# Kernel tuning notes

Measured on AMD Instinct MI355X. Metric: run time of the kernel, lower is better.

Reference implementation:

```python
import jax, jax.numpy as jnp
import numpy as np

B, F, V, E = 16384, 20, 100000, 32
D_BOT = F * E            # 640
DIMS = (512, 256)        # bottom MLP dims
TDIMS = (128, 64)        # tower hidden dims
N_DOM = 4


def setup_inputs() -> dict:
    key = jax.random.key(0)
    ks = jax.random.split(key, 16)
    inp = {
        "feature_ids": jax.random.randint(ks[0], (B, F), 0, V, dtype=jnp.int64),
        "domain_id": jax.random.randint(ks[1], (B,), 0, N_DOM, dtype=jnp.int64),
        # embedding tables [F, V, E]
        "emb": jax.random.normal(ks[2], (F, V, E), dtype=jnp.float32) * 0.01,
        # bottom MLP: 640 -> 512 -> 256 (relu, no output layer)
        "W1": jax.random.normal(ks[3], (D_BOT, DIMS[0]), dtype=jnp.float32) * (1.0 / np.sqrt(D_BOT)),
        "b1": jnp.zeros((DIMS[0],), dtype=jnp.float32),
        "W2": jax.random.normal(ks[4], (DIMS[0], DIMS[1]), dtype=jnp.float32) * (1.0 / np.sqrt(DIMS[0])),
        "b2": jnp.zeros((DIMS[1],), dtype=jnp.float32),
        # towers (stacked over domain dim): 256 -> 128 -> 64 -> 1
        "TW1": jax.random.normal(ks[5], (N_DOM, DIMS[1], TDIMS[0]), dtype=jnp.float32) * (1.0 / np.sqrt(DIMS[1])),
        "Tb1": jnp.zeros((N_DOM, TDIMS[0]), dtype=jnp.float32),
        "TW2": jax.random.normal(ks[6], (N_DOM, TDIMS[0], TDIMS[1]), dtype=jnp.float32) * (1.0 / np.sqrt(TDIMS[0])),
        "Tb2": jnp.zeros((N_DOM, TDIMS[1]), dtype=jnp.float32),
        "TW3": jax.random.normal(ks[7], (N_DOM, TDIMS[1], 1), dtype=jnp.float32) * (1.0 / np.sqrt(TDIMS[1])),
        "Tb3": jnp.zeros((N_DOM, 1), dtype=jnp.float32),
    }
    return inp


def reference(feature_ids, domain_id, emb, W1, b1, W2, b2, TW1, Tb1, TW2, Tb2, TW3, Tb3):
    # Embedding lookup + concat: [B, F, E] -> [B, F*E]
    e = emb[jnp.arange(F)[None, :], feature_ids]          # [B, F, E]
    h = e.reshape(B, F * E)
    # Shared bottom MLP (relu)
    h = jax.nn.relu(h @ W1 + b1)                          # [B, 512]
    h = jax.nn.relu(h @ W2 + b2)                          # [B, 256]
    # All domain towers computed densely for every sample (faithful to source)
    t = jax.nn.relu(jnp.einsum('bi,dio->bdo', h, TW1) + Tb1[None])   # [B, D, 128]
    t = jax.nn.relu(jnp.einsum('bdi,dio->bdo', t, TW2) + Tb2[None])  # [B, D, 64]
    logit = jnp.einsum('bdi,dio->bdo', t, TW3) + Tb3[None]           # [B, D, 1]
    ys = jax.nn.sigmoid(logit)[..., 0]                    # [B, D]
    # Select per-sample domain output via mask (domains are exclusive)
    onehot = jax.nn.one_hot(domain_id, N_DOM, dtype=ys.dtype)        # [B, D]
    final = jnp.sum(ys * onehot, axis=1)                  # [B]
    return final
```

## Files before the change

### kernel.cpp

```cpp
#include <hip/hip_runtime.h>

#define B_SZ  16384
#define F_SZ  20
#define V_SZ  100000
#define E_SZ  32
#define DBOT  640
#define D1    512
#define D2    256
#define T1D   128
#define T2D   64
#define NDOM  4

typedef __bf16 bf16x8 __attribute__((ext_vector_type(8)));
typedef float  f32x4  __attribute__((ext_vector_type(4)));

#define MFMA(a, b, c) __builtin_amdgcn_mfma_f32_16x16x32_bf16((a), (b), (c), 0, 0, 0)

__global__ __launch_bounds__(256) void k_prep(const float* __restrict__ W1,
                                              const float* __restrict__ W2,
                                              const float* __restrict__ TW1,
                                              const float* __restrict__ TW2,
                                              __bf16* __restrict__ W1P,
                                              __bf16* __restrict__ W2P,
                                              __bf16* __restrict__ TW1P,
                                              __bf16* __restrict__ TW2P) {
  int bid = blockIdx.x, tid = threadIdx.x;
  const float* src; __bf16* dst; int n, k, N;
  if (bid < 160) {
    long g = (long)bid * 256 + tid;
    int lane = g & 63; int kkg = (int)((g >> 6) % 20); int ntile = (int)(g / 1280);
    n = ntile * 16 + (lane & 15); k = kkg * 32 + ((lane >> 4) << 3);
    src = W1; N = D1; dst = W1P + g * 8;
  } else if (bid < 224) {
    long g = (long)(bid - 160) * 256 + tid;
    int lane = g & 63; int kkg = (int)((g >> 6) & 15); int ntile = (int)(g >> 10);
    n = ntile * 16 + (lane & 15); k = kkg * 32 + ((lane >> 4) << 3);
    src = W2; N = D2; dst = W2P + g * 8;
  } else if (bid < 288) {
    long g = (long)(bid - 224) * 256 + tid;
    int d = (int)(g >> 12); long r = g & 4095;
    int lane = r & 63; int kkg = (int)((r >> 6) & 7); int ntile = (int)(r >> 9);
    n = ntile * 16 + (lane & 15); k = kkg * 32 + ((lane >> 4) << 3);
    src = TW1 + (long)d * D2 * T1D; N = T1D;
    dst = TW1P + ((long)(d * 64 + ntile * 8 + kkg) * 64 + lane) * 8;
  } else {
    long g = (long)(bid - 288) * 256 + tid;
    int d = (int)(g >> 10); long r = g & 1023;
    int lane = r & 63; int kkg = (int)((r >> 6) & 3); int ntile = (int)(r >> 8);
    n = ntile * 16 + (lane & 15); k = kkg * 32 + ((lane >> 4) << 3);
    src = TW2 + (long)d * T1D * T2D; N = T2D;
    dst = TW2P + ((long)(d * 16 + ntile * 4 + kkg) * 64 + lane) * 8;
  }
  bf16x8 o;
#pragma unroll
  for (int e = 0; e < 8; ++e) o[e] = (__bf16)src[(long)(k + e) * N + n];
  *(bf16x8*)dst = o;
}

__global__ __launch_bounds__(512) void k_mega(const int* __restrict__ fids,
                                              const int* __restrict__ dom,
                                              const float* __restrict__ emb,
                                              const __bf16* __restrict__ W1P,
                                              const float* __restrict__ b1,
                                              const __bf16* __restrict__ W2P,
                                              const float* __restrict__ b2,
                                              const __bf16* __restrict__ TW1P,
                                              const __bf16* __restrict__ TW2P,
                                              const float* __restrict__ Tb1,
                                              const float* __restrict__ Tb2,
                                              const float* __restrict__ TW3,
                                              const float* __restrict__ Tb3,
                                              float* __restrict__ out) {
  __shared__ __attribute__((aligned(16))) char smem[152576];
  int*    ids_lds = (int*)(smem + 147456);
  __bf16* sA      = (__bf16*)smem;
  __bf16* h1      = (__bf16*)(smem + 81920);
  __bf16* h2_lds  = (__bf16*)smem;
  __bf16* t_lds   = (__bf16*)(smem + 81920);

  int bid = blockIdx.x, tid = threadIdx.x;
  int lane = tid & 63, w = tid >> 6;
  int lrow = lane & 15, kq = lane >> 4;
  int m0 = bid * 64;

  for (int i = tid; i < 64 * F_SZ; i += 512) ids_lds[i] = fids[m0 * F_SZ + i];
  __syncthreads();

  int row0 = tid >> 4,          cc0 = tid & 15;
  int row1 = (tid + 512) >> 4,  cc1 = tid & 15;
  int sb0 = (row0 * 1280 + cc0 * 16) ^ ((row0 & 7) << 4);
  int sb1 = (row1 * 1280 + cc1 * 16) ^ ((row1 & 7) << 4);
  int f0base = cc0 >> 2, es0 = (cc0 & 3) << 3;
  int f1base = cc1 >> 2, es1 = (cc1 & 3) << 3;

  float4 g0a, g0b, g1a, g1b;
  {
    int f = f0base;
    int id = ids_lds[row0 * F_SZ + f];
    const float* p = emb + ((long)f * V_SZ + id) * E_SZ + es0;
    g0a = *(const float4*)p; g0b = *(const float4*)(p + 4);
    f = f1base;
    id = ids_lds[row1 * F_SZ + f];
    const float* q = emb + ((long)f * V_SZ + id) * E_SZ + es1;
    g1a = *(const float4*)q; g1b = *(const float4*)(q + 4);
  }

  f32x4 acc[4][4] = {};

#pragma unroll
  for (int g = 0; g < 5; ++g) {
    {
      bf16x8 o;
      o[0] = (__bf16)g0a.x; o[1] = (__bf16)g0a.y; o[2] = (__bf16)g0a.z; o[3] = (__bf16)g0a.w;
      o[4] = (__bf16)g0b.x; o[5] = (__bf16)g0b.y; o[6] = (__bf16)g0b.z; o[7] = (__bf16)g0b.w;
      *(bf16x8*)((char*)sA + sb0 + g * 256) = o;
      o[0] = (__bf16)g1a.x; o[1] = (__bf16)g1a.y; o[2] = (__bf16)g1a.z; o[3] = (__bf16)g1a.w;
      o[4] = (__bf16)g1b.x; o[5] = (__bf16)g1b.y; o[6] = (__bf16)g1b.z; o[7] = (__bf16)g1b.w;
      *(bf16x8*)((char*)sA + sb1 + g * 256) = o;
    }
    asm volatile("s_waitcnt lgkmcnt(0)" ::: "memory");
    __builtin_amdgcn_s_barrier();
    __builtin_amdgcn_sched_barrier(0);

    bf16x8 bfr[4][4];
#pragma unroll
    for (int f4 = 0; f4 < 4; ++f4)
#pragma unroll
      for (int ni = 0; ni < 4; ++ni)
        bfr[f4][ni] = *(const bf16x8*)(W1P +
            ((long)((w * 4 + ni) * 20 + g * 4 + f4) * 64 + lane) * 8);
    __builtin_amdgcn_sched_barrier(0);

    if (g < 4) {
      int f = (g + 1) * 4 + f0base;
      int id = ids_lds[row0 * F_SZ + f];
      const float* p = emb + ((long)f * V_SZ + id) * E_SZ + es0;
      g0a = *(const float4*)p; g0b = *(const float4*)(p + 4);
      f = (g + 1) * 4 + f1base;
      id = ids_lds[row1 * F_SZ + f];
      const float* q = emb + ((long)f * V_SZ + id) * E_SZ + es1;
      g1a = *(const float4*)q; g1b = *(const float4*)(q + 4);
    }
    __builtin_amdgcn_sched_barrier(0);

#pragma unroll
    for (int f4 = 0; f4 < 4; ++f4) {
      int f = g * 4 + f4;
      bf16x8 af[4];
#pragma unroll
      for (int mi = 0; mi < 4; ++mi) {
        int byte = ((mi * 16 + lrow) * 1280 + (f * 32 + kq * 8) * 2) ^ ((lrow & 7) << 4);
        af[mi] = *(const bf16x8*)((const char*)sA + byte);
      }
#pragma unroll
      for (int ni = 0; ni < 4; ++ni)
#pragma unroll
        for (int mi = 0; mi < 4; ++mi)
          acc[mi][ni] = MFMA(af[mi], bfr[f4][ni], acc[mi][ni]);
    }
  }

#pragma unroll
  for (int ni = 0; ni < 4; ++ni) {
    int col = w * 64 + ni * 16 + lrow;
    float bv = b1[col];
#pragma unroll
    for (int mi = 0; mi < 4; ++mi) {
#pragma unroll
      for (int r = 0; r < 4; ++r) {
        int row = mi * 16 + kq * 4 + r;
        float v = acc[mi][ni][r] + bv;
        v = v > 0.f ? v : 0.f;
        int byte = (row * 1024 + col * 2) ^ ((row & 7) << 4);
        *(__bf16*)((char*)h1 + byte) = (__bf16)v;
      }
    }
  }
  __syncthreads();

  {
    f32x4 acc2[4][2] = {};
#pragma unroll 4
    for (int kkg = 0; kkg < 16; ++kkg) {
      bf16x8 a2[4];
#pragma unroll
      for (int mi = 0; mi < 4; ++mi) {
        int byte = ((mi * 16 + lrow) * 1024 + kkg * 64 + kq * 16) ^ ((lrow & 7) << 4);
        a2[mi] = *(const bf16x8*)((const char*)h1 + byte);
      }
#pragma unroll
      for (int ni = 0; ni < 2; ++ni) {
        bf16x8 bfr2 = *(const bf16x8*)(W2P +
            ((long)((w * 2 + ni) * 16 + kkg) * 64 + lane) * 8);
#pragma unroll
        for (int mi = 0; mi < 4; ++mi)
          acc2[mi][ni] = MFMA(a2[mi], bfr2, acc2[mi][ni]);
      }
    }
#pragma unroll
    for (int ni = 0; ni < 2; ++ni) {
      int col = w * 32 + ni * 16 + lrow;
      float bv = b2[col];
#pragma unroll
      for (int mi = 0; mi < 4; ++mi) {
#pragma unroll
        for (int r = 0; r < 4; ++r) {
          int row = mi * 16 + kq * 4 + r;
          float v = acc2[mi][ni][r] + bv;
          v = v > 0.f ? v : 0.f;
          int byte = (row * 512 + col * 2) ^ ((row & 7) << 4);
          *(__bf16*)((char*)h2_lds + byte) = (__bf16)v;
        }
      }
    }
  }
  __syncthreads();

  {
    int d  = w >> 1;
    int r0 = (w & 1) * 32;
    __bf16* tw = t_lds + w * 4096;

    bf16x8 a1[2][8];
#pragma unroll
    for (int mi = 0; mi < 2; ++mi)
#pragma unroll
      for (int kk = 0; kk < 8; ++kk) {
        int row = r0 + mi * 16 + lrow;
        int byte = (row * 512 + (kk * 32 + kq * 8) * 2) ^ ((row & 7) << 4);
        a1[mi][kk] = *(const bf16x8*)((const char*)h2_lds + byte);
      }

    f32x4 acc1[2][8] = {};
#pragma unroll
    for (int kk = 0; kk < 8; ++kk) {
#pragma unroll
      for (int ni = 0; ni < 8; ++ni) {
        bf16x8 b = *(const bf16x8*)(TW1P +
            ((long)(d * 64 + ni * 8 + kk) * 64 + lane) * 8);
#pragma unroll
        for (int mi = 0; mi < 2; ++mi)
          acc1[mi][ni] = MFMA(a1[mi][kk], b, acc1[mi][ni]);
      }
    }
#pragma unroll
    for (int ni = 0; ni < 8; ++ni) {
      float bv = Tb1[d * T1D + ni * 16 + lrow];
#pragma unroll
      for (int mi = 0; mi < 2; ++mi) {
#pragma unroll
        for (int r = 0; r < 4; ++r) {
          int lr = mi * 16 + kq * 4 + r;
          float v = acc1[mi][ni][r] + bv;
          v = v > 0.f ? v : 0.f;
          int byte = (lr * 256 + (ni * 16 + lrow) * 2) ^ ((lr & 7) << 4);
          *(__bf16*)((char*)tw + byte) = (__bf16)v;
        }
      }
    }
    asm volatile("s_waitcnt lgkmcnt(0)" ::: "memory");

    bf16x8 a2f[2][4];
#pragma unroll
    for (int mi = 0; mi < 2; ++mi)
#pragma unroll
      for (int kk = 0; kk < 4; ++kk) {
        int lr = mi * 16 + lrow;
        int byte = (lr * 256 + (kk * 32 + kq * 8) * 2) ^ ((lr & 7) << 4);
        a2f[mi][kk] = *(const bf16x8*)((const char*)tw + byte);
      }
    asm volatile("s_waitcnt lgkmcnt(0)" ::: "memory");
    f32x4 acc2[2][4] = {};
#pragma unroll
    for (int kk = 0; kk < 4; ++kk) {
#pragma unroll
      for (int ni = 0; ni < 4; ++ni) {
        bf16x8 b = *(const bf16x8*)(TW2P +
            ((long)(d * 16 + ni * 4 + kk) * 64 + lane) * 8);
#pragma unroll
        for (int mi = 0; mi < 2; ++mi)
          acc2[mi][ni] = MFMA(a2f[mi][kk], b, acc2[mi][ni]);
      }
    }
#pragma unroll
    for (int ni = 0; ni < 4; ++ni) {
      float bv = Tb2[d * T2D + ni * 16 + lrow];
#pragma unroll
      for (int mi = 0; mi < 2; ++mi) {
#pragma unroll
        for (int r = 0; r < 4; ++r) {
          int lr = mi * 16 + kq * 4 + r;
          float v = acc2[mi][ni][r] + bv;
          v = v > 0.f ? v : 0.f;
          int byte = (lr * 128 + (ni * 16 + lrow) * 2) ^ ((lr & 7) << 4);
          *(__bf16*)((char*)tw + byte) = (__bf16)v;
        }
      }
    }
    asm volatile("s_waitcnt lgkmcnt(0)" ::: "memory");

    {
      int lr    = (kq & 1) * 16 + lrow;
      int khalf = kq >> 1;
      float s = 0.f;
#pragma unroll
      for (int j = 0; j < 32; ++j) {
        int col = khalf * 32 + j;
        int byte = (lr * 128 + col * 2) ^ ((lr & 7) << 4);
        s += (float)*(const __bf16*)((const char*)tw + byte) * TW3[d * T2D + col];
      }
      s += __shfl_xor(s, 32);
      s += Tb3[d];
      int grow = r0 + lr;
      if (khalf == 0 && dom[m0 + grow] == d)
        out[m0 + grow] = 1.0f / (1.0f + expf(-s));
    }
  }
}

extern "C" void kernel_launch(void* const* d_in, const int* in_sizes, int n_in,
                              void* d_out, int out_size, void* d_ws, size_t ws_size,
                              hipStream_t stream) {
  const int*   fids = (const int*)d_in[0];
  const int*   dom  = (const int*)d_in[1];
  const float* emb  = (const float*)d_in[2];
  const float* W1   = (const float*)d_in[3];
  const float* b1   = (const float*)d_in[4];
  const float* W2   = (const float*)d_in[5];
  const float* b2   = (const float*)d_in[6];
  const float* TW1  = (const float*)d_in[7];
  const float* Tb1  = (const float*)d_in[8];
  const float* TW2  = (const float*)d_in[9];
  const float* Tb2  = (const float*)d_in[10];
  const float* TW3  = (const float*)d_in[11];
  const float* Tb3  = (const float*)d_in[12];
  float* out = (float*)d_out;

  char* ws = (char*)d_ws;
  __bf16* W1P   = (__bf16*)(ws);
  __bf16* W2P   = (__bf16*)(ws + 655360);
  __bf16* TW1P  = (__bf16*)(ws + 917504);
  __bf16* TW2P  = (__bf16*)(ws + 1179648);

  k_prep<<<304, 256, 0, stream>>>(W1, W2, TW1, TW2, W1P, W2P, TW1P, TW2P);
  k_mega<<<256, 512, 0, stream>>>(fids, dom, emb, W1P, b1, W2P, b2,
                                  TW1P, TW2P, Tb1, Tb2, TW3, Tb3, out);
}
```

Measured before the change: 44.10 us.

## Deepen embedding gather prefetch to three stages and use MFMA for final tower layer

The first-layer loop is unrolled by hand so embedding gathers run up to three groups ahead of the MFMA work instead of one, which hides more of the random-access gather latency. The weight fragment load for the next group is also issued right after the current MFMA block. Separately, the final 64->1 tower dot product now uses two bf16 MFMAs per row tile, with TW3 packed to bf16 in the prep kernel, replacing a scalar loop over LDS. The deeper prefetch keeps more float4 values live in registers, which raises register pressure, and the last layer now rounds TW3 to bf16.

```diff
diff --git a/kernel.cpp b/kernel.cpp
--- a/kernel.cpp
+++ b/kernel.cpp
@@ -20,10 +20,12 @@
                                               const float* __restrict__ W2,
                                               const float* __restrict__ TW1,
                                               const float* __restrict__ TW2,
+                                              const float* __restrict__ TW3,
                                               __bf16* __restrict__ W1P,
                                               __bf16* __restrict__ W2P,
                                               __bf16* __restrict__ TW1P,
-                                              __bf16* __restrict__ TW2P) {
+                                              __bf16* __restrict__ TW2P,
+                                              __bf16* __restrict__ TW3P) {
   int bid = blockIdx.x, tid = threadIdx.x;
   const float* src; __bf16* dst; int n, k, N;
   if (bid < 160) {
@@ -43,13 +45,16 @@
     n = ntile * 16 + (lane & 15); k = kkg * 32 + ((lane >> 4) << 3);
     src = TW1 + (long)d * D2 * T1D; N = T1D;
     dst = TW1P + ((long)(d * 64 + ntile * 8 + kkg) * 64 + lane) * 8;
-  } else {
+  } else if (bid < 304) {
     long g = (long)(bid - 288) * 256 + tid;
     int d = (int)(g >> 10); long r = g & 1023;
     int lane = r & 63; int kkg = (int)((r >> 6) & 3); int ntile = (int)(r >> 8);
     n = ntile * 16 + (lane & 15); k = kkg * 32 + ((lane >> 4) << 3);
     src = TW2 + (long)d * T1D * T2D; N = T2D;
     dst = TW2P + ((long)(d * 16 + ntile * 4 + kkg) * 64 + lane) * 8;
+  } else {
+    if (tid < NDOM * T2D) TW3P[tid] = (__bf16)TW3[tid];
+    return;
   }
   bf16x8 o;
 #pragma unroll
@@ -66,9 +71,9 @@
                                               const float* __restrict__ b2,
                                               const __bf16* __restrict__ TW1P,
                                               const __bf16* __restrict__ TW2P,
+                                              const __bf16* __restrict__ TW3P,
                                               const float* __restrict__ Tb1,
                                               const float* __restrict__ Tb2,
-                                              const float* __restrict__ TW3,
                                               const float* __restrict__ Tb3,
                                               float* __restrict__ out) {
   __shared__ __attribute__((aligned(16))) char smem[152576];
@@ -93,72 +98,94 @@
   int f0base = cc0 >> 2, es0 = (cc0 & 3) << 3;
   int f1base = cc1 >> 2, es1 = (cc1 & 3) << 3;
 
-  float4 g0a, g0b, g1a, g1b;
-  {
-    int f = f0base;
-    int id = ids_lds[row0 * F_SZ + f];
-    const float* p = emb + ((long)f * V_SZ + id) * E_SZ + es0;
-    g0a = *(const float4*)p; g0b = *(const float4*)(p + 4);
-    f = f1base;
-    id = ids_lds[row1 * F_SZ + f];
-    const float* q = emb + ((long)f * V_SZ + id) * E_SZ + es1;
-    g1a = *(const float4*)q; g1b = *(const float4*)(q + 4);
-  }
-
+#define GATHER(G, P0, P1, P2, P3)                                            \
+    { int f_ = (G) * 4 + f0base;                                             \
+      int id_ = ids_lds[row0 * F_SZ + f_];                                   \
+      const float* p_ = emb + ((long)f_ * V_SZ + id_) * E_SZ + es0;          \
+      P0 = *(const float4*)p_; P1 = *(const float4*)(p_ + 4);                \
+      f_ = (G) * 4 + f1base;                                                 \
+      id_ = ids_lds[row1 * F_SZ + f_];                                       \
+      const float* q_ = emb + ((long)f_ * V_SZ + id_) * E_SZ + es1;          \
+      P2 = *(const float4*)q_; P3 = *(const float4*)(q_ + 4); }
+
+#define COMMIT(S, P0, P1, P2, P3)                                            \
+    { bf16x8 o_;                                                             \
+      o_[0]=(__bf16)P0.x; o_[1]=(__bf16)P0.y; o_[2]=(__bf16)P0.z; o_[3]=(__bf16)P0.w; \
+      o_[4]=(__bf16)P1.x; o_[5]=(__bf16)P1.y; o_[6]=(__bf16)P1.z; o_[7]=(__bf16)P1.w; \
+      *(bf16x8*)((char*)sA + sb0 + (S) * 256) = o_;                          \
+      o_[0]=(__bf16)P2.x; o_[1]=(__bf16)P2.y; o_[2]=(__bf16)P2.z; o_[3]=(__bf16)P2.w; \
+      o_[4]=(__bf16)P3.x; o_[5]=(__bf16)P3.y; o_[6]=(__bf16)P3.z; o_[7]=(__bf16)P3.w; \
+      *(bf16x8*)((char*)sA + sb1 + (S) * 256) = o_; }
+
+#define BFRLOAD(G)                                                           \
+    _Pragma("unroll")                                                        \
+    for (int f4 = 0; f4 < 4; ++f4)                                           \
+      _Pragma("unroll")                                                      \
+      for (int ni = 0; ni < 4; ++ni)                                         \
+        bfr[f4][ni] = *(const bf16x8*)(W1P +                                 \
+            ((long)((w * 4 + ni) * 20 + (G) * 4 + f4) * 64 + lane) * 8);
+
+#define SYNCP()                                                              \
+    asm volatile("s_waitcnt lgkmcnt(0)" ::: "memory");                       \
+    __builtin_amdgcn_s_barrier();                                            \
+    __builtin_amdgcn_sched_barrier(0);
+
+#define MFMAG(G)                                                             \
+    _Pragma("unroll")                                                        \
+    for (int f4 = 0; f4 < 4; ++f4) {                                         \
+      int f_ = (G) * 4 + f4;                                                 \
+      bf16x8 af[4];                                                          \
+      _Pragma("unroll")                                                      \
+      for (int mi = 0; mi < 4; ++mi) {                                       \
+        int byte_ = ((mi * 16 + lrow) * 1280 + (f_ * 32 + kq * 8) * 2) ^ ((lrow & 7) << 4); \
+        af[mi] = *(const bf16x8*)((const char*)sA + byte_);                  \
+      }                                                                      \
+      _Pragma("unroll")                                                      \
+      for (int ni = 0; ni < 4; ++ni)                                         \
+        _Pragma("unroll")                                                    \
+        for (int mi = 0; mi < 4; ++mi)                                       \
+          acc[mi][ni] = MFMA(af[mi], bfr[f4][ni], acc[mi][ni]);              \
+    }
+
+  float4 xA0, xA1, xB0, xB1, yA0, yA1, yB0, yB1, zA0, zA1, zB0, zB1;
+  bf16x8 bfr[4][4];
   f32x4 acc[4][4] = {};
 
-#pragma unroll
-  for (int g = 0; g < 5; ++g) {
-    {
-      bf16x8 o;
-      o[0] = (__bf16)g0a.x; o[1] = (__bf16)g0a.y; o[2] = (__bf16)g0a.z; o[3] = (__bf16)g0a.w;
-      o[4] = (__bf16)g0b.x; o[5] = (__bf16)g0b.y; o[6] = (__bf16)g0b.z; o[7] = (__bf16)g0b.w;
-      *(bf16x8*)((char*)sA + sb0 + g * 256) = o;
-      o[0] = (__bf16)g1a.x; o[1] = (__bf16)g1a.y; o[2] = (__bf16)g1a.z; o[3] = (__bf16)g1a.w;
-      o[4] = (__bf16)g1b.x; o[5] = (__bf16)g1b.y; o[6] = (__bf16)g1b.z; o[7] = (__bf16)g1b.w;
-      *(bf16x8*)((char*)sA + sb1 + g * 256) = o;
-    }
-    asm volatile("s_waitcnt lgkmcnt(0)" ::: "memory");
-    __builtin_amdgcn_s_barrier();
-    __builtin_amdgcn_sched_barrier(0);
-
-    bf16x8 bfr[4][4];
-#pragma unroll
-    for (int f4 = 0; f4 < 4; ++f4)
-#pragma unroll
-      for (int ni = 0; ni < 4; ++ni)
-        bfr[f4][ni] = *(const bf16x8*)(W1P +
-            ((long)((w * 4 + ni) * 20 + g * 4 + f4) * 64 + lane) * 8);
-    __builtin_amdgcn_sched_barrier(0);
-
-    if (g < 4) {
-      int f = (g + 1) * 4 + f0base;
-      int id = ids_lds[row0 * F_SZ + f];
-      const float* p = emb + ((long)f * V_SZ + id) * E_SZ + es0;
-      g0a = *(const float4*)p; g0b = *(const float4*)(p + 4);
-      f = (g + 1) * 4 + f1base;
-      id = ids_lds[row1 * F_SZ + f];
-      const float* q = emb + ((long)f * V_SZ + id) * E_SZ + es1;
-      g1a = *(const float4*)q; g1b = *(const float4*)(q + 4);
-    }
-    __builtin_amdgcn_sched_barrier(0);
-
-#pragma unroll
-    for (int f4 = 0; f4 < 4; ++f4) {
-      int f = g * 4 + f4;
-      bf16x8 af[4];
-#pragma unroll
-      for (int mi = 0; mi < 4; ++mi) {
-        int byte = ((mi * 16 + lrow) * 1280 + (f * 32 + kq * 8) * 2) ^ ((lrow & 7) << 4);
-        af[mi] = *(const bf16x8*)((const char*)sA + byte);
-      }
-#pragma unroll
-      for (int ni = 0; ni < 4; ++ni)
-#pragma unroll
-        for (int mi = 0; mi < 4; ++mi)
-          acc[mi][ni] = MFMA(af[mi], bfr[f4][ni], acc[mi][ni]);
-    }
-  }
+  BFRLOAD(0)
+  __builtin_amdgcn_sched_barrier(0);
+  GATHER(0, xA0, xA1, xB0, xB1)
+  GATHER(1, yA0, yA1, yB0, yB1)
+  GATHER(2, zA0, zA1, zB0, zB1)
+
+  COMMIT(0, xA0, xA1, xB0, xB1)
+  SYNCP()
+  GATHER(3, xA0, xA1, xB0, xB1)
+  __builtin_amdgcn_sched_barrier(0);
+  MFMAG(0)
+  BFRLOAD(1)
+  COMMIT(1, yA0, yA1, yB0, yB1)
+  SYNCP()
+  GATHER(4, yA0, yA1, yB0, yB1)
+  __builtin_amdgcn_sched_barrier(0);
+  MFMAG(1)
+  BFRLOAD(2)
+  COMMIT(2, zA0, zA1, zB0, zB1)
+  SYNCP()
+  MFMAG(2)
+  BFRLOAD(3)
+  COMMIT(3, xA0, xA1, xB0, xB1)
+  SYNCP()
+  MFMAG(3)
+  BFRLOAD(4)
+  COMMIT(4, yA0, yA1, yB0, yB1)
+  SYNCP()
+  MFMAG(4)
+
+#undef GATHER
+#undef COMMIT
+#undef BFRLOAD
+#undef SYNCP
+#undef MFMAG
 
 #pragma unroll
   for (int ni = 0; ni < 4; ++ni) {
@@ -300,20 +327,31 @@
     asm volatile("s_waitcnt lgkmcnt(0)" ::: "memory");
 
     {
-      int lr    = (kq & 1) * 16 + lrow;
-      int khalf = kq >> 1;
-      float s = 0.f;
-#pragma unroll
-      for (int j = 0; j < 32; ++j) {
-        int col = khalf * 32 + j;
-        int byte = (lr * 128 + col * 2) ^ ((lr & 7) << 4);
-        s += (float)*(const __bf16*)((const char*)tw + byte) * TW3[d * T2D + col];
-      }
-      s += __shfl_xor(s, 32);
-      s += Tb3[d];
-      int grow = r0 + lr;
-      if (khalf == 0 && dom[m0 + grow] == d)
-        out[m0 + grow] = 1.0f / (1.0f + expf(-s));
+      bf16x8 b3_0 = *(const bf16x8*)(TW3P + d * 64 + kq * 8);
+      bf16x8 b3_1 = *(const bf16x8*)(TW3P + d * 64 + 32 + kq * 8);
+      f32x4 acc3[2] = {};
+#pragma unroll
+      for (int rt = 0; rt < 2; ++rt) {
+        int lr = rt * 16 + lrow;
+        int byte0 = (lr * 128 + (kq * 8) * 2) ^ ((lr & 7) << 4);
+        int byte1 = (lr * 128 + (32 + kq * 8) * 2) ^ ((lr & 7) << 4);
+        bf16x8 a3_0 = *(const bf16x8*)((const char*)tw + byte0);
+        bf16x8 a3_1 = *(const bf16x8*)((const char*)tw + byte1);
+        acc3[rt] = MFMA(a3_0, b3_0, acc3[rt]);
+        acc3[rt] = MFMA(a3_1, b3_1, acc3[rt]);
+      }
+      if (lrow == 0) {
+#pragma unroll
+        for (int rt = 0; rt < 2; ++rt)
+#pragma unroll
+          for (int r = 0; r < 4; ++r) {
+            int grow = r0 + rt * 16 + kq * 4 + r;
+            if (dom[m0 + grow] == d) {
+              float s = acc3[rt][r] + Tb3[d];
+              out[m0 + grow] = 1.0f / (1.0f + expf(-s));
+            }
+          }
+      }
     }
   }
 }
@@ -341,8 +379,10 @@
   __bf16* W2P   = (__bf16*)(ws + 655360);
   __bf16* TW1P  = (__bf16*)(ws + 917504);
   __bf16* TW2P  = (__bf16*)(ws + 1179648);
-
-  k_prep<<<304, 256, 0, stream>>>(W1, W2, TW1, TW2, W1P, W2P, TW1P, TW2P);
+  __bf16* TW3P  = (__bf16*)(ws + 1245184);
+
+  k_prep<<<305, 256, 0, stream>>>(W1, W2, TW1, TW2, TW3,
+                                  W1P, W2P, TW1P, TW2P, TW3P);
   k_mega<<<256, 512, 0, stream>>>(fids, dom, emb, W1P, b1, W2P, b2,
-                                  TW1P, TW2P, Tb1, Tb2, TW3, Tb3, out);
+                                  TW1P, TW2P, TW3P, Tb1, Tb2, Tb3, out);
 }
```

New measurement: 46.43 us. 5.3% more time.
